# Kernel tuning notes

Hardware: AMD Instinct MI355X
Metric: run time of the kernel (lower is better)

The kernel has to match this reference:

```python
import jax, jax.numpy as jnp
import numpy as np

B = 128        # graphs per batch
N = 512        # nodes per graph (all graphs full-size)
F = 128        # input/hidden feature dim
DEG_AVG = 16   # average degree
E = B * N * DEG_AVG
DEGREES = (3, 3)  # polynomial filter order per conv layer


def setup_inputs() -> dict:
    key = jax.random.key(0)
    ks = jax.random.split(key, 8)
    X = jax.random.normal(ks[0], (B * N, F), dtype=jnp.float32)
    batch = jnp.repeat(jnp.arange(B, dtype=jnp.int32), N)
    # edges constrained within each graph: graph id = e // (N*DEG_AVG)
    gid = jnp.repeat(jnp.arange(B, dtype=jnp.int32), N * DEG_AVG)
    src = jax.random.randint(ks[1], (E,), 0, N, dtype=jnp.int32) + gid * N
    dst = jax.random.randint(ks[2], (E,), 0, N, dtype=jnp.int32) + gid * N
    edge_index = jnp.stack([src, dst], axis=0)
    s = 1.0 / np.sqrt(F)
    W1 = jax.random.normal(ks[3], (F, F), dtype=jnp.float32) * s
    b1 = jnp.zeros((F,), dtype=jnp.float32)
    W2 = jax.random.normal(ks[4], (F, F), dtype=jnp.float32) * s
    b2 = jnp.zeros((F,), dtype=jnp.float32)
    Wr1 = jax.random.normal(ks[5], (F, 64), dtype=jnp.float32) * s
    br1 = jnp.zeros((64,), dtype=jnp.float32)
    Wr2 = jax.random.normal(ks[6], (64, 1), dtype=jnp.float32) * (1.0 / 8.0)
    br2 = jnp.zeros((1,), dtype=jnp.float32)
    return {"X": X, "batch": batch, "edge_index": edge_index,
            "W1": W1, "b1": b1, "W2": W2, "b2": b2,
            "Wr1": Wr1, "br1": br1, "Wr2": Wr2, "br2": br2}


def _build_gso(edge_index):
    # dense per-graph adjacency [B, N, N] (block-diagonal global GSO,
    # represented batched for efficiency)
    g = edge_index[0] // N
    si = edge_index[0] % N
    di = edge_index[1] % N
    A = jnp.zeros((B, N, N), dtype=jnp.float32).at[g, si, di].set(1.0)
    # gso_generator: symmetric degree-normalized adjacency D^-1/2 A D^-1/2
    deg = A.sum(axis=-1)
    dinv = jnp.where(deg > 0, jax.lax.rsqrt(jnp.maximum(deg, 1e-12)), 0.0)
    S = dinv[:, :, None] * A * dinv[:, None, :]
    return S


def _poly_conv(S, x, degree, W, b):
    # sum_{k=0..degree} S^k x, then linear projection
    acc = x
    z = x
    for _ in range(degree):
        z = jnp.einsum('bij,bjf->bif', S, z)
        acc = acc + z
    return jnp.einsum('bnf,fo->bno', acc, W) + b


def reference(X, batch, edge_index, W1, b1, W2, b2, Wr1, br1, Wr2, br2):
    S = _build_gso(edge_index)
    x = X.reshape(B, N, F)  # nodes grouped per graph (batch is sorted)
    x = jax.nn.relu(_poly_conv(S, x, DEGREES[0], W1, b1))
    x = jax.nn.relu(_poly_conv(S, x, DEGREES[1], W2, b2))
    # global mean pool over nodes of each graph
    h = x.mean(axis=1)  # [B, F]
    h = jax.nn.relu(h @ Wr1 + br1)
    out = (h @ Wr2 + br2).squeeze(-1)  # [B]
    return out
```

## Files before the change

### kernel.cpp

```cpp
#include <hip/hip_runtime.h>
#include <hip/hip_bf16.h>

#define NB 128
#define NN 512
#define NF 128
#define BN (NB*NN)
#define NE (BN*16)
#define EPG 8192
#define WPR 16
#define ELLW 64
#define QST 32
#define SST 72
#define WTS 136

typedef short sh8 __attribute__((ext_vector_type(8)));
typedef float f32x4 __attribute__((ext_vector_type(4)));

static __device__ __forceinline__ unsigned short f2bf(float f) {
    unsigned u = __float_as_uint(f);
    u += 0x7fffu + ((u >> 16) & 1u);
    return (unsigned short)(u >> 16);
}

#define DOT2LO(acc_, pk_, one_) \
    asm("v_dot2_f32_bf16 %0, %1, %2, %0" : "+v"(acc_) : "v"(pk_), "v"(one_))

__global__ __launch_bounds__(256) void scatter_bitmap_kernel(
    const int* __restrict__ src, const int* __restrict__ dst,
    unsigned* __restrict__ bmg)
{
    __shared__ unsigned bm[128 * WPR];
    int b = blockIdx.x;
    int g = b >> 2;
    int qr = b & 3;
    int t = threadIdx.x;

    for (int i = t; i < 128 * WPR; i += 256) bm[i] = 0u;
    __syncthreads();

    const int4* sg4 = (const int4*)(src + (size_t)g * EPG);
    const int4* dg4 = (const int4*)(dst + (size_t)g * EPG);
    int lo = qr << 7;
    for (int i = t; i < EPG / 4; i += 256) {
        int4 s4 = sg4[i];
        int4 d4 = dg4[i];
        int s, d;
        s = s4.x & (NN - 1); d = d4.x & (NN - 1);
        if ((s >> 7) == qr) atomicOr(&bm[(s - lo) * WPR + (d >> 5)], 1u << (d & 31));
        s = s4.y & (NN - 1); d = d4.y & (NN - 1);
        if ((s >> 7) == qr) atomicOr(&bm[(s - lo) * WPR + (d >> 5)], 1u << (d & 31));
        s = s4.z & (NN - 1); d = d4.z & (NN - 1);
        if ((s >> 7) == qr) atomicOr(&bm[(s - lo) * WPR + (d >> 5)], 1u << (d & 31));
        s = s4.w & (NN - 1); d = d4.w & (NN - 1);
        if ((s >> 7) == qr) atomicOr(&bm[(s - lo) * WPR + (d >> 5)], 1u << (d & 31));
    }
    __syncthreads();

    unsigned* outg = bmg + ((size_t)g * NN + (size_t)qr * 128) * WPR;
    #pragma unroll
    for (int i = t; i < 128 * WPR / 4; i += 256)
        *(uint4*)&outg[i * 4] = *(const uint4*)&bm[i * 4];
}

__global__ __launch_bounds__(1024) void rank_ell_kernel(
    const unsigned* __restrict__ bmg,
    unsigned short* __restrict__ ell, int* __restrict__ ocnt,
    float* __restrict__ dinvr, int* __restrict__ perm)
{
    __shared__ unsigned short els[NN * SST];
    __shared__ int cs[NN];
    __shared__ int rdeg[NN];
    __shared__ int irank[NN];
    __shared__ int half1[NN];
    __shared__ int half2[NN];
    __shared__ int prk[NN];
    int g = blockIdx.x;
    int t = threadIdx.x;
    int row = t & 511;
    int hb  = t >> 9;
    int wo  = hb * 8;

    const unsigned* bgr = bmg + ((size_t)g * NN + row) * WPR + wo;
    uint4 q0 = *(const uint4*)bgr;
    uint4 q1 = *(const uint4*)(bgr + 4);
    unsigned rw[8] = {q0.x, q0.y, q0.z, q0.w, q1.x, q1.y, q1.z, q1.w};

    int pc = 0;
    #pragma unroll
    for (int w = 0; w < 8; ++w) pc += __popc(rw[w]);
    if (hb) half2[row] = pc; else half1[row] = pc;
    __syncthreads();

    if (!hb) {
        int d0 = pc + half2[row];
        if (d0 > ELLW) d0 = ELLW;
        cs[row] = d0;
    }
    __syncthreads();

    int deg_r = cs[row];
    {
        const int4* c4 = (const int4*)cs;
        int ib = hb * 64;
        int pcnt = 0;
        #pragma unroll 8
        for (int ii = 0; ii < 64; ++ii) {
            int4 v = c4[ib + ii];
            int i0 = (ib + ii) * 4;
            pcnt += (v.x < deg_r) || (v.x == deg_r && (i0 + 0) < row);
            pcnt += (v.y < deg_r) || (v.y == deg_r && (i0 + 1) < row);
            pcnt += (v.z < deg_r) || (v.z == deg_r && (i0 + 2) < row);
            pcnt += (v.w < deg_r) || (v.w == deg_r && (i0 + 3) < row);
        }
        if (!hb) prk[row] = pcnt;
        __syncthreads();
        if (hb) {
            int rk = prk[row] + pcnt;
            irank[row] = rk;
            rdeg[rk] = deg_r;
            perm[(size_t)g * NN + rk] = row;
            dinvr[(size_t)g * NN + rk] =
                (deg_r > 0) ? rsqrtf((float)deg_r) : 0.0f;
        }
    }
    __syncthreads();

    if (t < NN / 8) {
        int m = rdeg[t * 8 + 7];
        ocnt[(size_t)g * (NN / 8) + t] = (m + 3) & ~3;
    }

    {
        int rk = irank[row];
        unsigned short* er = &els[rk * SST];
        int c = hb ? half1[row] : 0;
        #pragma unroll
        for (int w = 0; w < 8; ++w) {
            unsigned bits = rw[w];
            while (bits) {
                int j = __ffs(bits) - 1;
                bits &= bits - 1;
                if (c < ELLW) er[c] = (unsigned short)irank[(wo + w) * 32 + j];
                ++c;
            }
        }
        if (hb) {
            if (c > ELLW) c = ELLW;
            for (int p = c; p < ELLW; ++p) er[p] = (unsigned short)NN;
        }
    }
    __syncthreads();

    unsigned short* outb = ell + (size_t)g * NN * ELLW;
    for (int idx = t; idx < NN * 8; idx += 1024) {
        int r2 = idx >> 3, sg2 = idx & 7;
        uint4 v = *(const uint4*)&els[r2 * SST + sg2 * 8];
        *(uint4*)&outb[(size_t)r2 * ELLW + sg2 * 8] = v;
    }
}

__global__ __launch_bounds__(512, 4) void poly_fused_kernel(
    const float* __restrict__ xin,
    unsigned short* __restrict__ accout,
    const unsigned short* __restrict__ ell,
    const int* __restrict__ ocnt,
    const float* __restrict__ dinvr,
    const int* __restrict__ perm,
    int permuteIn)
{
    extern __shared__ float lds[];
    unsigned short* w = (unsigned short*)lds;
    float* dsh = lds + ((NN + 1) * QST * 2) / 4;

    int b = blockIdx.x;
    int g = b & 127;
    int q = b >> 7;
    int t = threadIdx.x;
    int wid = t >> 6;
    int qd  = (t >> 2) & 15;
    int fbq = t & 3;

    unsigned one_lo = 0x00003F80u;
    unsigned one_hi = 0x3F800000u;

    if (t < NN) dsh[t] = dinvr[(size_t)g * NN + t];
    if (t < QST) w[NN * QST + t] = 0;

    int rnk[4];
    #pragma unroll
    for (int x = 0; x < 4; ++x) {
        int wl = (x >= 2) ? (7 - wid) : wid;
        rnk[x] = x * 128 + wl * 16 + qd;
    }

    const int* oc = ocnt + (size_t)g * (NN / 8);
    int co[4];
    #pragma unroll
    for (int x = 0; x < 4; ++x) {
        int ob = (rnk[x] - qd) >> 3;
        co[x] = __builtin_amdgcn_readfirstlane(max(oc[ob], oc[ob + 1]));
    }

    int px[4];
    if (permuteIn) {
        const int* pmg = perm + (size_t)g * NN;
        #pragma unroll
        for (int x = 0; x < 4; ++x) px[x] = pmg[rnk[x]];
    } else {
        #pragma unroll
        for (int x = 0; x < 4; ++x) px[x] = rnk[x];
    }

    const float* xg = xin + (size_t)g * NN * NF + q * 32 + fbq * 8;

    float acc[4][8];
    #pragma unroll
    for (int x = 0; x < 4; ++x) {
        int row = px[x];
        float4 a0 = *(const float4*)&xg[(size_t)row * NF];
        float4 a1 = *(const float4*)&xg[(size_t)row * NF + 4];
        acc[x][0] = a0.x; acc[x][1] = a0.y; acc[x][2] = a0.z; acc[x][3] = a0.w;
        acc[x][4] = a1.x; acc[x][5] = a1.y; acc[x][6] = a1.z; acc[x][7] = a1.w;
    }

    __syncthreads();

    #pragma unroll
    for (int x = 0; x < 4; ++x) {
        float di = dsh[rnk[x]];
        unsigned pk[4];
        #pragma unroll
        for (int k = 0; k < 4; ++k) {
            unsigned lo = (unsigned)f2bf(di * acc[x][2 * k]);
            unsigned hi = (unsigned)f2bf(di * acc[x][2 * k + 1]);
            pk[k] = lo | (hi << 16);
        }
        *(uint4*)&w[rnk[x] * QST + fbq * 8] = make_uint4(pk[0], pk[1], pk[2], pk[3]);
    }
    __syncthreads();

    for (int hop = 0; hop < 3; ++hop) {
        unsigned pst[4][4];
        #pragma unroll
        for (int x = 0; x < 4; ++x) {
            const unsigned short* el =
                ell + ((size_t)g * NN + rnk[x]) * ELLW;
            int cnt = co[x];
            float s[8];
            #pragma unroll
            for (int k = 0; k < 8; ++k) s[k] = 0.0f;

            ushort4 cur = *(const ushort4*)el;
            for (int p = 0; p < cnt; p += 4) {
                ushort4 nxt = cur;
                if (p + 4 < cnt) nxt = *(const ushort4*)(el + p + 4);
                uint4 v0 = *(const uint4*)&w[(int)cur.x * QST + fbq * 8];
                uint4 v1 = *(const uint4*)&w[(int)cur.y * QST + fbq * 8];
                uint4 v2 = *(const uint4*)&w[(int)cur.z * QST + fbq * 8];
                uint4 v3 = *(const uint4*)&w[(int)cur.w * QST + fbq * 8];
                unsigned d[4][4] = {{v0.x, v0.y, v0.z, v0.w},
                                    {v1.x, v1.y, v1.z, v1.w},
                                    {v2.x, v2.y, v2.z, v2.w},
                                    {v3.x, v3.y, v3.z, v3.w}};
                #pragma unroll
                for (int n = 0; n < 4; ++n) {
                    #pragma unroll
                    for (int k = 0; k < 4; ++k) {
                        DOT2LO(s[2 * k],     d[n][k], one_lo);
                        DOT2LO(s[2 * k + 1], d[n][k], one_hi);
                    }
                }
                cur = nxt;
            }

            float di = dsh[rnk[x]];
            #pragma unroll
            for (int k = 0; k < 4; ++k) {
                float zlo = di * s[2 * k];
                float zhi = di * s[2 * k + 1];
                acc[x][2 * k]     += zlo;
                acc[x][2 * k + 1] += zhi;
                unsigned lo = (unsigned)f2bf(di * zlo);
                unsigned hi = (unsigned)f2bf(di * zhi);
                pst[x][k] = lo | (hi << 16);
            }
        }
        __syncthreads();
        #pragma unroll
        for (int x = 0; x < 4; ++x) {
            *(uint4*)&w[rnk[x] * QST + fbq * 8] =
                make_uint4(pst[x][0], pst[x][1], pst[x][2], pst[x][3]);
        }
        __syncthreads();
    }

    unsigned short* og = accout + (size_t)g * NN * NF + q * 32 + fbq * 8;
    #pragma unroll
    for (int x = 0; x < 4; ++x) {
        int rr = rnk[x];
        uint4 pk;
        pk.x = (unsigned)f2bf(acc[x][0]) | ((unsigned)f2bf(acc[x][1]) << 16);
        pk.y = (unsigned)f2bf(acc[x][2]) | ((unsigned)f2bf(acc[x][3]) << 16);
        pk.z = (unsigned)f2bf(acc[x][4]) | ((unsigned)f2bf(acc[x][5]) << 16);
        pk.w = (unsigned)f2bf(acc[x][6]) | ((unsigned)f2bf(acc[x][7]) << 16);
        *(uint4*)&og[(size_t)rr * NF] = pk;
    }
}

__global__ __launch_bounds__(256, 2) void gemm_bias_relu_kernel(
    const unsigned short* __restrict__ X,
    const float* __restrict__ W,
    const float* __restrict__ b, float* __restrict__ Y,
    float* __restrict__ partial, int fuse)
{
    __shared__ __align__(16) unsigned short Wt[NF * WTS];
    __shared__ float part[4 * NF];

    int t = threadIdx.x;

    for (int i = t; i < NF * NF / 4; i += 256) {
        int k = i >> 5;
        int n4 = (i & 31) * 4;
        float4 wv = ((const float4*)W)[i];
        Wt[(n4 + 0) * WTS + k] = f2bf(wv.x);
        Wt[(n4 + 1) * WTS + k] = f2bf(wv.y);
        Wt[(n4 + 2) * WTS + k] = f2bf(wv.z);
        Wt[(n4 + 3) * WTS + k] = f2bf(wv.w);
    }
    __syncthreads();

    int lane = t & 63;
    int wid  = t >> 6;
    int quad = lane >> 4;
    int l16  = lane & 15;
    int rowA0 = blockIdx.x * 128 + wid * 32;

    union { uint4 q; sh8 v; } af[2][4];
    #pragma unroll
    for (int m = 0; m < 2; ++m) {
        int r = rowA0 + m * 16 + l16;
        const unsigned short* xr = X + (size_t)r * NF + quad * 8;
        #pragma unroll
        for (int kk = 0; kk < 4; ++kk)
            af[m][kk].q = *(const uint4*)(xr + kk * 32);
    }

    f32x4 acc[2][8];
    #pragma unroll
    for (int m = 0; m < 2; ++m)
        #pragma unroll
        for (int c = 0; c < 8; ++c) acc[m][c] = (f32x4){0.f, 0.f, 0.f, 0.f};

    #pragma unroll
    for (int c = 0; c < 8; ++c) {
        const unsigned short* wb = &Wt[(c * 16 + l16) * WTS + quad * 8];
        #pragma unroll
        for (int kk = 0; kk < 4; ++kk) {
            union { uint4 q; sh8 v; } bf_;
            bf_.q = *(const uint4*)(wb + kk * 32);
            acc[0][c] = __builtin_amdgcn_mfma_f32_16x16x32_bf16(
                af[0][kk].v, bf_.v, acc[0][c], 0, 0, 0);
            acc[1][c] = __builtin_amdgcn_mfma_f32_16x16x32_bf16(
                af[1][kk].v, bf_.v, acc[1][c], 0, 0, 0);
        }
    }

    float psum[8];
    #pragma unroll
    for (int c = 0; c < 8; ++c) psum[c] = 0.0f;

    #pragma unroll
    for (int c = 0; c < 8; ++c) {
        int col = c * 16 + l16;
        float bias = b[col];
        #pragma unroll
        for (int m = 0; m < 2; ++m) {
            #pragma unroll
            for (int reg = 0; reg < 4; ++reg) {
                int r = rowA0 + m * 16 + quad * 4 + reg;
                float v = fmaxf(acc[m][c][reg] + bias, 0.0f);
                if (!fuse) Y[(size_t)r * NF + col] = v;
                psum[c] += v;
            }
        }
    }

    if (fuse) {
        #pragma unroll
        for (int c = 0; c < 8; ++c) {
            float v = psum[c];
            v += __shfl_xor(v, 16);
            v += __shfl_xor(v, 32);
            if (lane < 16) part[wid * NF + c * 16 + lane] = v;
        }
        __syncthreads();
        if (t < NF) {
            float s = part[t] + part[NF + t] + part[2 * NF + t]
                    + part[3 * NF + t];
            partial[(size_t)blockIdx.x * NF + t] = s;
        }
    }
}

__global__ __launch_bounds__(128) void readout_kernel(
    const float* __restrict__ partial,
    const float* __restrict__ Wr1, const float* __restrict__ br1,
    const float* __restrict__ Wr2, const float* __restrict__ br2,
    float* __restrict__ out)
{
    __shared__ float hsh[NF];
    __shared__ float r1[64];

    int g = blockIdx.x;
    int t = threadIdx.x;

    const float* pg = partial + (size_t)g * 4 * NF;
    float s = 0.0f;
    #pragma unroll
    for (int j = 0; j < 4; ++j) s += pg[j * NF + t];
    hsh[t] = s * (1.0f / (float)NN);
    __syncthreads();

    if (t < 64) {
        float a = br1[t];
        #pragma unroll 8
        for (int k = 0; k < NF; ++k) a += hsh[k] * Wr1[k * 64 + t];
        r1[t] = fmaxf(a, 0.0f);
    }
    __syncthreads();

    if (t < 64) {
        float v = r1[t] * Wr2[t];
        #pragma unroll
        for (int off = 32; off; off >>= 1) v += __shfl_down(v, off);
        if (t == 0) out[g] = v + br2[0];
    }
}

extern "C" void kernel_launch(void* const* d_in, const int* in_sizes, int n_in,
                              void* d_out, int out_size, void* d_ws, size_t ws_size,
                              hipStream_t stream)
{
    const float* X    = (const float*)d_in[0];
    const int*   ei   = (const int*)d_in[2];
    const float* W1   = (const float*)d_in[3];
    const float* b1   = (const float*)d_in[4];
    const float* W2   = (const float*)d_in[5];
    const float* b2   = (const float*)d_in[6];
    const float* Wr1  = (const float*)d_in[7];
    const float* br1  = (const float*)d_in[8];
    const float* Wr2  = (const float*)d_in[9];
    const float* br2  = (const float*)d_in[10];
    float* out = (float*)d_out;

    const int* src = ei;
    const int* dst = ei + NE;

    char* ws = (char*)d_ws;
    float*          dinvr   = (float*)(ws);
    int*            ocnt    = (int*)(ws + (size_t)256 * 1024);
    int*            perm    = (int*)(ws + (size_t)512 * 1024);
    float*          partial = (float*)(ws + (size_t)768 * 1024);
    unsigned short* ell     = (unsigned short*)(ws + (size_t)1024 * 1024);
    unsigned*       bmg     = (unsigned*)(ws + (size_t)9216 * 1024);
    unsigned short* buf0    = (unsigned short*)(ws + (size_t)16384 * 1024);
    float*          buf1    = (float*)(ws + (size_t)49152 * 1024);

    scatter_bitmap_kernel<<<NB * 4, 256, 0, stream>>>(src, dst, bmg);
    rank_ell_kernel<<<NB, 1024, 0, stream>>>(bmg, ell, ocnt, dinvr, perm);

    const size_t LDSSZ = (size_t)(NN + 1) * QST * 2 + NN * 4;

    poly_fused_kernel<<<NB * 4, 512, LDSSZ, stream>>>(X, buf0, ell, ocnt,
                                                      dinvr, perm, 1);
    gemm_bias_relu_kernel<<<BN / 128, 256, 0, stream>>>(buf0, W1, b1, buf1,
                                                        partial, 0);

    poly_fused_kernel<<<NB * 4, 512, LDSSZ, stream>>>(buf1, buf0, ell, ocnt,
                                                      dinvr, perm, 0);
    gemm_bias_relu_kernel<<<BN / 128, 256, 0, stream>>>(buf0, W2, b2, buf1,
                                                        partial, 1);

    readout_kernel<<<NB, 128, 0, stream>>>(partial, Wr1, br1, Wr2, br2, out);
}
```

Measured before the change: 220.3 us.

## Split rank/ELL build across two blocks per graph with quarter-row threads

```diff
diff --git a/kernel.cpp b/kernel.cpp
--- a/kernel.cpp
+++ b/kernel.cpp
@@ -67,92 +67,100 @@
     unsigned short* __restrict__ ell, int* __restrict__ ocnt,
     float* __restrict__ dinvr, int* __restrict__ perm)
 {
-    __shared__ unsigned short els[NN * SST];
+    __shared__ unsigned short els[256 * SST];
+    __shared__ int qp[NN * 4];
     __shared__ int cs[NN];
     __shared__ int rdeg[NN];
     __shared__ int irank[NN];
-    __shared__ int half1[NN];
-    __shared__ int half2[NN];
+    __shared__ int prow[NN];
     __shared__ int prk[NN];
-    int g = blockIdx.x;
+    int b = blockIdx.x;
+    int g = b >> 1;
+    int h = b & 1;
     int t = threadIdx.x;
-    int row = t & 511;
-    int hb  = t >> 9;
-    int wo  = hb * 8;
-
-    const unsigned* bgr = bmg + ((size_t)g * NN + row) * WPR + wo;
-    uint4 q0 = *(const uint4*)bgr;
-    uint4 q1 = *(const uint4*)(bgr + 4);
-    unsigned rw[8] = {q0.x, q0.y, q0.z, q0.w, q1.x, q1.y, q1.z, q1.w};
-
-    int pc = 0;
-    #pragma unroll
-    for (int w = 0; w < 8; ++w) pc += __popc(rw[w]);
-    if (hb) half2[row] = pc; else half1[row] = pc;
-    __syncthreads();
-
-    if (!hb) {
-        int d0 = pc + half2[row];
-        if (d0 > ELLW) d0 = ELLW;
-        cs[row] = d0;
-    }
-    __syncthreads();
-
-    int deg_r = cs[row];
+
     {
+        int r = t & 511, hf = t >> 9;
+        const unsigned* bgr = bmg + ((size_t)g * NN + r) * WPR + hf * 8;
+        uint4 a = *(const uint4*)bgr;
+        uint4 c = *(const uint4*)(bgr + 4);
+        qp[r * 4 + hf * 2]     = __popc(a.x) + __popc(a.y) + __popc(a.z) + __popc(a.w);
+        qp[r * 4 + hf * 2 + 1] = __popc(c.x) + __popc(c.y) + __popc(c.z) + __popc(c.w);
+    }
+    __syncthreads();
+    if (t < NN) {
+        int d = qp[t * 4] + qp[t * 4 + 1] + qp[t * 4 + 2] + qp[t * 4 + 3];
+        cs[t] = (d > ELLW) ? ELLW : d;
+    }
+    __syncthreads();
+
+    {
+        int r = t & 511, hf = t >> 9;
+        int deg_r = cs[r];
         const int4* c4 = (const int4*)cs;
-        int ib = hb * 64;
+        int ib = hf * 64;
         int pcnt = 0;
         #pragma unroll 8
         for (int ii = 0; ii < 64; ++ii) {
             int4 v = c4[ib + ii];
             int i0 = (ib + ii) * 4;
-            pcnt += (v.x < deg_r) || (v.x == deg_r && (i0 + 0) < row);
-            pcnt += (v.y < deg_r) || (v.y == deg_r && (i0 + 1) < row);
-            pcnt += (v.z < deg_r) || (v.z == deg_r && (i0 + 2) < row);
-            pcnt += (v.w < deg_r) || (v.w == deg_r && (i0 + 3) < row);
-        }
-        if (!hb) prk[row] = pcnt;
+            pcnt += (v.x < deg_r) || (v.x == deg_r && (i0 + 0) < r);
+            pcnt += (v.y < deg_r) || (v.y == deg_r && (i0 + 1) < r);
+            pcnt += (v.z < deg_r) || (v.z == deg_r && (i0 + 2) < r);
+            pcnt += (v.w < deg_r) || (v.w == deg_r && (i0 + 3) < r);
+        }
+        if (!hf) prk[r] = pcnt;
         __syncthreads();
-        if (hb) {
-            int rk = prk[row] + pcnt;
-            irank[row] = rk;
+        if (hf) {
+            int rk = prk[r] + pcnt;
+            irank[r] = rk;
             rdeg[rk] = deg_r;
-            perm[(size_t)g * NN + rk] = row;
-            dinvr[(size_t)g * NN + rk] =
-                (deg_r > 0) ? rsqrtf((float)deg_r) : 0.0f;
-        }
-    }
-    __syncthreads();
-
-    if (t < NN / 8) {
+            prow[rk] = r;
+            if (h == 0) {
+                perm[(size_t)g * NN + rk] = r;
+                dinvr[(size_t)g * NN + rk] =
+                    (deg_r > 0) ? rsqrtf((float)deg_r) : 0.0f;
+            }
+        }
+    }
+    __syncthreads();
+
+    if (h == 0 && t < NN / 8) {
         int m = rdeg[t * 8 + 7];
         ocnt[(size_t)g * (NN / 8) + t] = (m + 3) & ~3;
     }
 
     {
-        int rk = irank[row];
-        unsigned short* er = &els[rk * SST];
-        int c = hb ? half1[row] : 0;
-        #pragma unroll
-        for (int w = 0; w < 8; ++w) {
-            unsigned bits = rw[w];
+        int rkl = t >> 2;
+        int qw  = t & 3;
+        int rk  = h * 256 + rkl;
+        int row = prow[rk];
+        const unsigned* bq = bmg + ((size_t)g * NN + row) * WPR + qw * 4;
+        uint4 bv = *(const uint4*)bq;
+        unsigned wbits[4] = {bv.x, bv.y, bv.z, bv.w};
+        int c = 0;
+        #pragma unroll
+        for (int j = 0; j < 3; ++j) c += (j < qw) ? qp[row * 4 + j] : 0;
+        unsigned short* er = &els[rkl * SST];
+        #pragma unroll
+        for (int w = 0; w < 4; ++w) {
+            unsigned bits = wbits[w];
             while (bits) {
                 int j = __ffs(bits) - 1;
                 bits &= bits - 1;
-                if (c < ELLW) er[c] = (unsigned short)irank[(wo + w) * 32 + j];
+                if (c < ELLW) er[c] = (unsigned short)irank[(qw * 4 + w) * 32 + j];
                 ++c;
             }
         }
-        if (hb) {
-            if (c > ELLW) c = ELLW;
-            for (int p = c; p < ELLW; ++p) er[p] = (unsigned short)NN;
-        }
-    }
-    __syncthreads();
-
-    unsigned short* outb = ell + (size_t)g * NN * ELLW;
-    for (int idx = t; idx < NN * 8; idx += 1024) {
+        if (qw == 3) {
+            int cc = (c > ELLW) ? ELLW : c;
+            for (int p = cc; p < ELLW; ++p) er[p] = (unsigned short)NN;
+        }
+    }
+    __syncthreads();
+
+    unsigned short* outb = ell + ((size_t)g * NN + (size_t)h * 256) * ELLW;
+    for (int idx = t; idx < 256 * 8; idx += 1024) {
         int r2 = idx >> 3, sg2 = idx & 7;
         uint4 v = *(const uint4*)&els[r2 * SST + sg2 * 8];
         *(uint4*)&outb[(size_t)r2 * ELLW + sg2 * 8] = v;
@@ -467,7 +475,7 @@
     float*          buf1    = (float*)(ws + (size_t)49152 * 1024);
 
     scatter_bitmap_kernel<<<NB * 4, 256, 0, stream>>>(src, dst, bmg);
-    rank_ell_kernel<<<NB, 1024, 0, stream>>>(bmg, ell, ocnt, dinvr, perm);
+    rank_ell_kernel<<<NB * 2, 1024, 0, stream>>>(bmg, ell, ocnt, dinvr, perm);
 
     const size_t LDSSZ = (size_t)(NN + 1) * QST * 2 + NN * 4;
 
```

Result: no change. 218.2 us (-0.9%).
